# Optimization experiments

Measured on AMD Instinct MI355X. Metric: run time of the kernel, lower is better.

Reference implementation:

```python
import jax, jax.numpy as jnp
import numpy as np

B, S, HID = 4, 2048, 2048
NH, NKV, HD = 16, 4, 128  # query heads, kv heads, head_dim


def setup_inputs() -> dict:
    key = jax.random.key(0)
    ks = jax.random.split(key, 7)
    scale = 1.0 / np.sqrt(HID)
    x = jax.random.normal(ks[0], (B, S, HID), dtype=jnp.float32)
    # rope tables (interleaved-pair convention matching rotate_half)
    inv_freq = 1.0 / (1000000.0 ** (np.arange(0, HD, 2, dtype=np.float32) / HD))
    t = np.arange(S, dtype=np.float32)
    freqs = np.outer(t, inv_freq)                      # (S, HD/2)
    emb = np.repeat(freqs, 2, axis=-1)                 # (S, HD) interleaved
    cos = jnp.asarray(np.cos(emb))
    sin = jnp.asarray(np.sin(emb))
    wq = jax.random.normal(ks[1], (HID, NH * HD), dtype=jnp.float32) * scale
    wk = jax.random.normal(ks[2], (HID, NKV * HD), dtype=jnp.float32) * scale
    wv = jax.random.normal(ks[3], (HID, NKV * HD), dtype=jnp.float32) * scale
    wo = jax.random.normal(ks[4], (NH * HD, HID), dtype=jnp.float32) * scale
    return {"x": x, "cos": cos, "sin": sin, "wq": wq, "wk": wk, "wv": wv, "wo": wo}


def _rotate_half(u):
    even = u[..., ::2]
    odd = u[..., 1::2]
    return jnp.stack((-odd, even), axis=-1).reshape(u.shape)


def reference(x, cos, sin, wq, wk, wv, wo):
    b, s, _ = x.shape
    rep = NH // NKV
    q = (x @ wq).reshape(b, s, NH, HD)
    k = (x @ wk).reshape(b, s, NKV, HD)
    v = (x @ wv).reshape(b, s, NKV, HD)
    # RoPE: cos/sin (S, HD) -> broadcast over batch and heads (unsqueeze_dim=1)
    c = cos[:s][None, :, None, :]
    sn = sin[:s][None, :, None, :]
    q = q * c + _rotate_half(q) * sn
    k = k * c + _rotate_half(k) * sn
    # GQA: group query heads per kv head; avoid materializing repeated K/V
    q = q.transpose(0, 2, 1, 3).reshape(b, NKV, rep, s, HD)   # (b, kv, rep, s, d)
    k = k.transpose(0, 2, 1, 3)                                # (b, kv, s, d)
    v = v.transpose(0, 2, 1, 3)                                # (b, kv, s, d)
    scores = jnp.einsum("bgrqd,bgkd->bgrqk", q, k) / jnp.sqrt(jnp.float32(HD))
    causal = jnp.tril(jnp.ones((s, s), dtype=bool))
    scores = jnp.where(causal, scores, jnp.finfo(scores.dtype).min)
    probs = jax.nn.softmax(scores, axis=-1)
    out = jnp.einsum("bgrqk,bgkd->bgrqd", probs, v)            # (b, kv, rep, s, d)
    out = out.reshape(b, NH, s, HD).transpose(0, 2, 1, 3).reshape(b, s, NH * HD)
    return out @ wo
```

## Files before the change

kernel.cpp:

```cpp
#include <hip/hip_runtime.h>

#define HIDD 2048
#define SEQ  2048
#define BATCH 4
#define NHQ  16
#define NKVH 4
#define HDIM 128
#define QKVN 3072

typedef unsigned short u16;
typedef unsigned int   u32;
using bf16x8 = __attribute__((ext_vector_type(8))) __bf16;
using u16x8  = __attribute__((ext_vector_type(8))) u16;
using u16x4  = __attribute__((ext_vector_type(4))) u16;
using f32x4  = __attribute__((ext_vector_type(4))) float;

__device__ __forceinline__ float bf2f(u16 v){ u32 u = ((u32)v) << 16; float f; __builtin_memcpy(&f, &u, 4); return f; }
__device__ __forceinline__ u16 f2bf(float f){ u32 u; __builtin_memcpy(&u, &f, 4); u += 0x7fffu + ((u >> 16) & 1u); return (u16)(u >> 16); }

__device__ __forceinline__ void gl_lds16(const void* g, void* l){
  __builtin_amdgcn_global_load_lds((const __attribute__((address_space(1))) void*)g,
                                   (__attribute__((address_space(3))) void*)l, 16, 0, 0);
}


__global__ void cvt_f32_bf16(const float* __restrict__ in, u16* __restrict__ out, int n4){
  int i = blockIdx.x * 256 + threadIdx.x;
  if (i >= n4) return;
  float4 v = ((const float4*)in)[i];
  u16x4 o; o[0] = f2bf(v.x); o[1] = f2bf(v.y); o[2] = f2bf(v.z); o[3] = f2bf(v.w);
  ((u16x4*)out)[i] = o;
}

__global__ void transpose_cvt_f32(const float* __restrict__ in, u16* __restrict__ out, int R, int C){
  __shared__ float t[32][33];
  int c0 = blockIdx.x * 32, r0 = blockIdx.y * 32;
  int tx = threadIdx.x, ty = threadIdx.y;
  #pragma unroll
  for (int i = 0; i < 4; i++)
    t[ty + 8*i][tx] = in[(size_t)(r0 + ty + 8*i) * C + c0 + tx];
  __syncthreads();
  #pragma unroll
  for (int i = 0; i < 4; i++)
    out[(size_t)(c0 + ty + 8*i) * R + r0 + tx] = f2bf(t[tx][ty + 8*i]);
}

__global__ void transpose_v(const u16* __restrict__ V, u16* __restrict__ Vt, int ld, int voff){
  __shared__ u16 t[32][33];
  int bg = blockIdx.z;
  int b = bg >> 2, g = bg & 3;
  const u16* in = V + (size_t)b * SEQ * ld + voff + g * HDIM;
  u16* out = Vt + (size_t)bg * HDIM * SEQ;
  int c0 = blockIdx.x * 32, r0 = blockIdx.y * 32;
  int tx = threadIdx.x, ty = threadIdx.y;
  #pragma unroll
  for (int i = 0; i < 4; i++)
    t[ty + 8*i][tx] = in[(size_t)(r0 + ty + 8*i) * ld + c0 + tx];
  __syncthreads();
  #pragma unroll
  for (int i = 0; i < 4; i++)
    out[(size_t)(c0 + ty + 8*i) * SEQ + r0 + tx] = t[tx][ty + 8*i];
}

__global__ void rope_kernel(u16* __restrict__ X, int ld, int ncl,
                            const float* __restrict__ ct, const float* __restrict__ st,
                            float scale, int n8){
  int i = blockIdx.x * 256 + threadIdx.x;
  if (i >= n8) return;
  int e0 = i * 8;
  int row = e0 >> ncl;
  int col = e0 & ((1 << ncl) - 1);
  int pos = row & (SEQ - 1);
  int dd  = col & (HDIM - 1);
  u16* p = X + (size_t)row * ld + col;
  u16x8 v = *(const u16x8*)p;
  const float* cp = ct + (size_t)pos * HDIM + dd;
  const float* sp = st + (size_t)pos * HDIM + dd;
  float f[8];
  #pragma unroll
  for (int j = 0; j < 8; j++) f[j] = bf2f(v[j]);
  u16x8 o;
  #pragma unroll
  for (int j = 0; j < 8; j += 2){
    float c = cp[j], s = sp[j];
    float e = f[j], od = f[j+1];
    o[j]   = f2bf((e * c - od * s) * scale);
    o[j+1] = f2bf((od * c + e * s) * scale);
  }
  *(u16x8*)p = o;
}

template<int OUT_BF16>
__global__ __launch_bounds__(256) void gemm_bt(const u16* __restrict__ A, const u16* __restrict__ Bt,
                                               void* __restrict__ Cv, int M, int N, int K){
  __shared__ __align__(16) u16 As[128*32];
  __shared__ __align__(16) u16 Bs[128*32];
  const int tid = threadIdx.x;
  const int wid = tid >> 6, lane = tid & 63;
  const int lr = lane & 15, lk = lane >> 4;
  const int m0 = blockIdx.y * 128, n0 = blockIdx.x * 128;
  const int wr = (wid >> 1) * 64, wc = (wid & 1) * 64;

  f32x4 acc[4][4];
  #pragma unroll
  for (int m = 0; m < 4; m++)
    #pragma unroll
    for (int n = 0; n < 4; n++) acc[m][n] = f32x4{0.f,0.f,0.f,0.f};

  const int srow = lane >> 2;
  const int swz  = ((lane & 3) * 8) ^ ((srow & 3) * 8);
  const u16* Ag = A  + (size_t)(m0 + wid*32 + srow) * K + swz;
  const u16* Bg = Bt + (size_t)(n0 + wid*32 + srow) * K + swz;
  u16* Asl = As + wid * 1024;
  u16* Bsl = Bs + wid * 1024;
  const int rsw = (lr & 3) * 8;

  for (int k0 = 0; k0 < K; k0 += 32){
    gl_lds16(Ag + k0,          Asl);
    gl_lds16(Ag + k0 + 16*K,   Asl + 512);
    gl_lds16(Bg + k0,          Bsl);
    gl_lds16(Bg + k0 + 16*K,   Bsl + 512);
    __syncthreads();
    bf16x8 a[4], b[4];
    #pragma unroll
    for (int m = 0; m < 4; m++) a[m] = *(const bf16x8*)&As[(wr + m*16 + lr)*32 + ((lk*8) ^ rsw)];
    #pragma unroll
    for (int n = 0; n < 4; n++) b[n] = *(const bf16x8*)&Bs[(wc + n*16 + lr)*32 + ((lk*8) ^ rsw)];
    #pragma unroll
    for (int m = 0; m < 4; m++)
      #pragma unroll
      for (int n = 0; n < 4; n++)
        acc[m][n] = __builtin_amdgcn_mfma_f32_16x16x32_bf16(a[m], b[n], acc[m][n], 0, 0, 0);
    __syncthreads();
  }
  #pragma unroll
  for (int m = 0; m < 4; m++)
    #pragma unroll
    for (int n = 0; n < 4; n++)
      #pragma unroll
      for (int i = 0; i < 4; i++){
        int gr = m0 + wr + m*16 + lk*4 + i;
        int gc = n0 + wc + n*16 + lr;
        float v = acc[m][n][i];
        if (OUT_BF16) ((u16*)Cv)[(size_t)gr * N + gc] = f2bf(v);
        else          ((float*)Cv)[(size_t)gr * N + gc] = v;
      }
}

__global__ __launch_bounds__(256) void attn_kernel(const u16* __restrict__ QKV, const u16* __restrict__ Vt,
                                                   u16* __restrict__ O){
  const int qt = (gridDim.x - 1) - blockIdx.x;
  const int h = blockIdx.y, b = blockIdx.z;
  const int g = h >> 2;
  const int tid = threadIdx.x;
  const int wid = tid >> 6, lane = tid & 63;
  const int lr = lane & 15, lk = lane >> 4;
  const int q0 = qt * 64;

  __shared__ __align__(16) u16 Ks[2][64*128];
  __shared__ __align__(16) u16 Vs[2][128*64];
  __shared__ __align__(16) u16 Ps[4][16*72];

  bf16x8 qf[4];
  {
    const int qrow = q0 + wid*16 + lr;
    const u16* qp = QKV + (size_t)(b*SEQ + qrow) * QKVN + h*HDIM + lk*8;
    #pragma unroll
    for (int c = 0; c < 4; c++) qf[c] = *(const bf16x8*)(qp + c*32);
  }

  const u16* Kbase = QKV + (size_t)b * SEQ * QKVN + HIDD + g*HDIM;
  const u16* Vbase = Vt + (size_t)(b*NKVH + g) * HDIM * SEQ;
  const int klr = lane >> 4, kj = lane & 15;
  const int vlr = lane >> 3, vj = lane & 7;

  #define STAGE(buf, t) do {                                                        \
    int kv0_ = (t) * 64;                                                            \
    _Pragma("unroll")                                                               \
    for (int iw = 0; iw < 4; iw++){                                                 \
      int kcb = wid*4 + iw;                                                         \
      int r   = kcb*4 + klr;                                                        \
      gl_lds16(Kbase + (size_t)(kv0_ + r) * QKVN + ((kj ^ (r & 7)) << 3),           \
               &Ks[buf][kcb << 9]);                                                 \
      int d   = kcb*8 + vlr;                                                        \
      gl_lds16(Vbase + (size_t)d * SEQ + kv0_ + ((vj ^ (d & 7)) << 3),              \
               &Vs[buf][kcb << 9]);                                                 \
    }                                                                               \
  } while (0)

  f32x4 oacc[8];
  #pragma unroll
  for (int f = 0; f < 8; f++) oacc[f] = f32x4{0.f,0.f,0.f,0.f};
  float m_i[4], l_i[4];
  #pragma unroll
  for (int i = 0; i < 4; i++){ m_i[i] = -1e30f; l_i[i] = 0.f; }

  const int nt = qt + 1;
  int cur = 0;
  STAGE(0, 0);
  for (int t = 0; t < nt; ++t){
    __syncthreads();
    if (t + 1 < nt) STAGE(cur ^ 1, t + 1);

    const int kv0 = t * 64;
    f32x4 sf[4];
    #pragma unroll
    for (int n = 0; n < 4; n++){
      f32x4 a = f32x4{0.f,0.f,0.f,0.f};
      #pragma unroll
      for (int c = 0; c < 4; c++){
        bf16x8 kf = *(const bf16x8*)&Ks[cur][(n*16 + lr)*128 + (((c*4 + lk) ^ (lr & 7)) << 3)];
        a = __builtin_amdgcn_mfma_f32_16x16x32_bf16(qf[c], kf, a, 0, 0, 0);
      }
      sf[n] = a;
    }
    if (t == nt - 1){
      #pragma unroll
      for (int n = 0; n < 4; n++)
        #pragma unroll
        for (int i = 0; i < 4; i++){
          int kvg = kv0 + n*16 + lr;
          int qg  = q0 + wid*16 + lk*4 + i;
          if (kvg > qg) sf[n][i] = -1e30f;
        }
    }
    float rm[4];
    #pragma unroll
    for (int i = 0; i < 4; i++) rm[i] = fmaxf(fmaxf(sf[0][i], sf[1][i]), fmaxf(sf[2][i], sf[3][i]));
    #pragma unroll
    for (int off = 1; off < 16; off <<= 1)
      #pragma unroll
      for (int i = 0; i < 4; i++) rm[i] = fmaxf(rm[i], __shfl_xor(rm[i], off));

    int defer = 1;
    #pragma unroll
    for (int i = 0; i < 4; i++) defer &= (rm[i] <= m_i[i] + 11.5f);

    float p[4][4], rs[4];
    if (__all(defer)){
      #pragma unroll
      for (int i = 0; i < 4; i++){
        float s0 = 0.f;
        #pragma unroll
        for (int n = 0; n < 4; n++){ float pv = exp2f(sf[n][i] - m_i[i]); p[n][i] = pv; s0 += pv; }
        rs[i] = s0;
      }
    } else {
      #pragma unroll
      for (int i = 0; i < 4; i++){
        float mn = fmaxf(m_i[i], rm[i]);
        float cf = exp2f(m_i[i] - mn);
        float s0 = 0.f;
        #pragma unroll
        for (int n = 0; n < 4; n++){ float pv = exp2f(sf[n][i] - mn); p[n][i] = pv; s0 += pv; }
        rs[i] = s0; m_i[i] = mn; l_i[i] *= cf;
        #pragma unroll
        for (int f = 0; f < 8; f++) oacc[f][i] *= cf;
      }
    }
    #pragma unroll
    for (int off = 1; off < 16; off <<= 1)
      #pragma unroll
      for (int i = 0; i < 4; i++) rs[i] += __shfl_xor(rs[i], off);
    #pragma unroll
    for (int i = 0; i < 4; i++) l_i[i] += rs[i];

    #pragma unroll
    for (int n = 0; n < 4; n++)
      #pragma unroll
      for (int i = 0; i < 4; i++)
        Ps[wid][(lk*4 + i)*72 + n*16 + lr] = f2bf(p[n][i]);

    #pragma unroll
    for (int kc = 0; kc < 2; kc++){
      bf16x8 pf = *(const bf16x8*)&Ps[wid][lr*72 + kc*32 + lk*8];
      #pragma unroll
      for (int f = 0; f < 8; f++){
        bf16x8 vf = *(const bf16x8*)&Vs[cur][(f*16 + lr)*64 + (((kc*4 + lk) ^ (lr & 7)) << 3)];
        oacc[f] = __builtin_amdgcn_mfma_f32_16x16x32_bf16(pf, vf, oacc[f], 0, 0, 0);
      }
    }
    cur ^= 1;
  }
  #undef STAGE
  #pragma unroll
  for (int f = 0; f < 8; f++)
    #pragma unroll
    for (int i = 0; i < 4; i++){
      int qr = q0 + wid*16 + lk*4 + i;
      float v = oacc[f][i] / l_i[i];
      O[(size_t)(b*SEQ + qr) * (NHQ*HDIM) + h*HDIM + f*16 + lr] = f2bf(v);
    }
}


extern "C" void kernel_launch(void* const* d_in, const int* in_sizes, int n_in,
                              void* d_out, int out_size, void* d_ws, size_t ws_size,
                              hipStream_t stream){
  const float* x    = (const float*)d_in[0];
  const float* cosb = (const float*)d_in[1];
  const float* sinb = (const float*)d_in[2];
  const float* wq   = (const float*)d_in[3];
  const float* wk   = (const float*)d_in[4];
  const float* wv   = (const float*)d_in[5];
  const float* wo   = (const float*)d_in[6];
  float* out = (float*)d_out;

  char* ws = (char*)d_ws;
  u16* XB    = (u16*)(ws);
  u16* WQKVT = (u16*)(ws + 33554432);
  u16* WOT   = (u16*)(ws + 46137344);
  u16* QKV   = (u16*)(ws + 54525952);
  u16* VT    = (u16*)(ws + 104857600);

  dim3 tb(32, 8);
  cvt_f32_bf16<<<(BATCH*SEQ*HIDD/4 + 255)/256, 256, 0, stream>>>(x, XB, BATCH*SEQ*HIDD/4);
  transpose_cvt_f32<<<dim3(HIDD/32, HIDD/32), tb, 0, stream>>>(wq, WQKVT, HIDD, NHQ*HDIM);
  transpose_cvt_f32<<<dim3((NKVH*HDIM)/32, HIDD/32), tb, 0, stream>>>(wk, WQKVT + (size_t)2048*2048, HIDD, NKVH*HDIM);
  transpose_cvt_f32<<<dim3((NKVH*HDIM)/32, HIDD/32), tb, 0, stream>>>(wv, WQKVT + (size_t)2560*2048, HIDD, NKVH*HDIM);
  transpose_cvt_f32<<<dim3(HIDD/32, HIDD/32), tb, 0, stream>>>(wo, WOT, NHQ*HDIM, HIDD);
  gemm_bt<1><<<dim3(QKVN/128, BATCH*SEQ/128), 256, 0, stream>>>(XB, WQKVT, QKV, BATCH*SEQ, QKVN, HIDD);
  rope_kernel<<<(BATCH*SEQ*2048/8)/256, 256, 0, stream>>>(QKV, QKVN, 11, cosb, sinb, 0.12753165651003169f, BATCH*SEQ*2048/8);
  rope_kernel<<<(BATCH*SEQ*512/8)/256, 256, 0, stream>>>(QKV + HIDD, QKVN, 9, cosb, sinb, 1.0f, BATCH*SEQ*512/8);
  transpose_v<<<dim3(HDIM/32, SEQ/32, BATCH*NKVH), tb, 0, stream>>>(QKV, VT, QKVN, 2560);
  attn_kernel<<<dim3(SEQ/64, NHQ, BATCH), 256, 0, stream>>>(QKV, VT, XB);
  gemm_bt<0><<<dim3(HIDD/128, BATCH*SEQ/128), 256, 0, stream>>>(XB, WOT, out, BATCH*SEQ, HIDD, NHQ*HDIM);
}
```

Baseline: 758.2 us.

## Enlarge attention query tile to 128 rows with two 16-row subtiles per wave

Each block now handles 128 query rows, and each wave handles 32 rows as two 16-row subtiles. Every K/V tile staged into LDS is therefore reused across twice as many queries, and the K fragments read from LDS are shared by both subtiles. The QK MFMA is transposed (K as the A operand) so each lane owns one query row, which reduces the row max and row sum to two cross-lane shuffles. K/V staging pointers are precomputed and incremented, and fully masked tiles are skipped per wave. In exchange the grid has half as many blocks, each wave holds more registers, and causal work is less balanced within a block.

```diff
diff --git a/kernel.cpp b/kernel.cpp
--- a/kernel.cpp
+++ b/kernel.cpp
@@ -155,142 +155,162 @@
   const int tid = threadIdx.x;
   const int wid = tid >> 6, lane = tid & 63;
   const int lr = lane & 15, lk = lane >> 4;
-  const int q0 = qt * 64;
+  const int q0 = qt * 128;
+  const int q0w = q0 + wid * 32;
 
   __shared__ __align__(16) u16 Ks[2][64*128];
   __shared__ __align__(16) u16 Vs[2][128*64];
   __shared__ __align__(16) u16 Ps[4][16*72];
-
-  bf16x8 qf[4];
-  {
-    const int qrow = q0 + wid*16 + lr;
-    const u16* qp = QKV + (size_t)(b*SEQ + qrow) * QKVN + h*HDIM + lk*8;
-    #pragma unroll
-    for (int c = 0; c < 4; c++) qf[c] = *(const bf16x8*)(qp + c*32);
-  }
-
-  const u16* Kbase = QKV + (size_t)b * SEQ * QKVN + HIDD + g*HDIM;
-  const u16* Vbase = Vt + (size_t)(b*NKVH + g) * HDIM * SEQ;
+  u16* Pw = &Ps[wid][0];
+
+  bf16x8 qf[2][4];
+  #pragma unroll
+  for (int qh = 0; qh < 2; qh++){
+    const u16* qp = QKV + (size_t)(b*SEQ + q0w + qh*16 + lr) * QKVN + h*HDIM + lk*8;
+    #pragma unroll
+    for (int c = 0; c < 4; c++) qf[qh][c] = *(const bf16x8*)(qp + c*32);
+  }
+
   const int klr = lane >> 4, kj = lane & 15;
   const int vlr = lane >> 3, vj = lane & 7;
-
-  #define STAGE(buf, t) do {                                                        \
-    int kv0_ = (t) * 64;                                                            \
-    _Pragma("unroll")                                                               \
-    for (int iw = 0; iw < 4; iw++){                                                 \
-      int kcb = wid*4 + iw;                                                         \
-      int r   = kcb*4 + klr;                                                        \
-      gl_lds16(Kbase + (size_t)(kv0_ + r) * QKVN + ((kj ^ (r & 7)) << 3),           \
-               &Ks[buf][kcb << 9]);                                                 \
-      int d   = kcb*8 + vlr;                                                        \
-      gl_lds16(Vbase + (size_t)d * SEQ + kv0_ + ((vj ^ (d & 7)) << 3),              \
-               &Vs[buf][kcb << 9]);                                                 \
-    }                                                                               \
-  } while (0)
-
-  f32x4 oacc[8];
-  #pragma unroll
-  for (int f = 0; f < 8; f++) oacc[f] = f32x4{0.f,0.f,0.f,0.f};
-  float m_i[4], l_i[4];
-  #pragma unroll
-  for (int i = 0; i < 4; i++){ m_i[i] = -1e30f; l_i[i] = 0.f; }
-
-  const int nt = qt + 1;
+  const u16* Kst[4]; const u16* Vst[4];
+  {
+    const u16* Kbase = QKV + (size_t)b * SEQ * QKVN + HIDD + g*HDIM;
+    const u16* Vbase = Vt + (size_t)(b*NKVH + g) * HDIM * SEQ;
+    #pragma unroll
+    for (int iw = 0; iw < 4; iw++){
+      int kcb = wid*4 + iw;
+      int r   = kcb*4 + klr;
+      Kst[iw] = Kbase + (size_t)r * QKVN + ((kj ^ (r & 7)) << 3);
+      int d   = kcb*8 + vlr;
+      Vst[iw] = Vbase + (size_t)d * SEQ + ((vj ^ (d & 7)) << 3);
+    }
+  }
+
+  f32x4 oacc[2][8];
+  #pragma unroll
+  for (int qh = 0; qh < 2; qh++)
+    #pragma unroll
+    for (int f = 0; f < 8; f++) oacc[qh][f] = f32x4{0.f,0.f,0.f,0.f};
+  float m_i[2] = {-1e30f, -1e30f}, l_i[2] = {0.f, 0.f};
+
+  const int nt = 2 * (qt + 1);
   int cur = 0;
-  STAGE(0, 0);
+  #pragma unroll
+  for (int iw = 0; iw < 4; iw++){
+    int kcb = wid*4 + iw;
+    gl_lds16(Kst[iw], &Ks[0][kcb << 9]);
+    gl_lds16(Vst[iw], &Vs[0][kcb << 9]);
+    Kst[iw] += 64 * QKVN;
+    Vst[iw] += 64;
+  }
+
   for (int t = 0; t < nt; ++t){
     __syncthreads();
-    if (t + 1 < nt) STAGE(cur ^ 1, t + 1);
-
+    if (t + 1 < nt){
+      #pragma unroll
+      for (int iw = 0; iw < 4; iw++){
+        int kcb = wid*4 + iw;
+        gl_lds16(Kst[iw], &Ks[cur ^ 1][kcb << 9]);
+        gl_lds16(Vst[iw], &Vs[cur ^ 1][kcb << 9]);
+        Kst[iw] += 64 * QKVN;
+        Vst[iw] += 64;
+      }
+    }
     const int kv0 = t * 64;
-    f32x4 sf[4];
-    #pragma unroll
-    for (int n = 0; n < 4; n++){
-      f32x4 a = f32x4{0.f,0.f,0.f,0.f};
-      #pragma unroll
-      for (int c = 0; c < 4; c++){
-        bf16x8 kf = *(const bf16x8*)&Ks[cur][(n*16 + lr)*128 + (((c*4 + lk) ^ (lr & 7)) << 3)];
-        a = __builtin_amdgcn_mfma_f32_16x16x32_bf16(qf[c], kf, a, 0, 0, 0);
-      }
-      sf[n] = a;
-    }
-    if (t == nt - 1){
-      #pragma unroll
-      for (int n = 0; n < 4; n++)
-        #pragma unroll
-        for (int i = 0; i < 4; i++){
-          int kvg = kv0 + n*16 + lr;
-          int qg  = q0 + wid*16 + lk*4 + i;
-          if (kvg > qg) sf[n][i] = -1e30f;
+    if (kv0 <= q0w + 31){
+      f32x4 sf[2][4];
+      #pragma unroll
+      for (int n = 0; n < 4; n++){
+        bf16x8 kf[4];
+        #pragma unroll
+        for (int c = 0; c < 4; c++)
+          kf[c] = *(const bf16x8*)&Ks[cur][(n*16 + lr)*128 + (((c*4 + lk) ^ (lr & 7)) << 3)];
+        #pragma unroll
+        for (int qh = 0; qh < 2; qh++){
+          f32x4 a = f32x4{0.f,0.f,0.f,0.f};
+          #pragma unroll
+          for (int c = 0; c < 4; c++)
+            a = __builtin_amdgcn_mfma_f32_16x16x32_bf16(kf[c], qf[qh][c], a, 0, 0, 0);
+          sf[qh][n] = a;
         }
-    }
-    float rm[4];
-    #pragma unroll
-    for (int i = 0; i < 4; i++) rm[i] = fmaxf(fmaxf(sf[0][i], sf[1][i]), fmaxf(sf[2][i], sf[3][i]));
-    #pragma unroll
-    for (int off = 1; off < 16; off <<= 1)
-      #pragma unroll
-      for (int i = 0; i < 4; i++) rm[i] = fmaxf(rm[i], __shfl_xor(rm[i], off));
-
-    int defer = 1;
-    #pragma unroll
-    for (int i = 0; i < 4; i++) defer &= (rm[i] <= m_i[i] + 11.5f);
-
-    float p[4][4], rs[4];
-    if (__all(defer)){
-      #pragma unroll
-      for (int i = 0; i < 4; i++){
-        float s0 = 0.f;
-        #pragma unroll
-        for (int n = 0; n < 4; n++){ float pv = exp2f(sf[n][i] - m_i[i]); p[n][i] = pv; s0 += pv; }
-        rs[i] = s0;
-      }
-    } else {
-      #pragma unroll
-      for (int i = 0; i < 4; i++){
-        float mn = fmaxf(m_i[i], rm[i]);
-        float cf = exp2f(m_i[i] - mn);
-        float s0 = 0.f;
-        #pragma unroll
-        for (int n = 0; n < 4; n++){ float pv = exp2f(sf[n][i] - mn); p[n][i] = pv; s0 += pv; }
-        rs[i] = s0; m_i[i] = mn; l_i[i] *= cf;
-        #pragma unroll
-        for (int f = 0; f < 8; f++) oacc[f][i] *= cf;
-      }
-    }
-    #pragma unroll
-    for (int off = 1; off < 16; off <<= 1)
-      #pragma unroll
-      for (int i = 0; i < 4; i++) rs[i] += __shfl_xor(rs[i], off);
-    #pragma unroll
-    for (int i = 0; i < 4; i++) l_i[i] += rs[i];
-
-    #pragma unroll
-    for (int n = 0; n < 4; n++)
-      #pragma unroll
-      for (int i = 0; i < 4; i++)
-        Ps[wid][(lk*4 + i)*72 + n*16 + lr] = f2bf(p[n][i]);
-
-    #pragma unroll
-    for (int kc = 0; kc < 2; kc++){
-      bf16x8 pf = *(const bf16x8*)&Ps[wid][lr*72 + kc*32 + lk*8];
-      #pragma unroll
-      for (int f = 0; f < 8; f++){
-        bf16x8 vf = *(const bf16x8*)&Vs[cur][(f*16 + lr)*64 + (((kc*4 + lk) ^ (lr & 7)) << 3)];
-        oacc[f] = __builtin_amdgcn_mfma_f32_16x16x32_bf16(pf, vf, oacc[f], 0, 0, 0);
+      }
+      if (kv0 + 63 > q0w){
+        #pragma unroll
+        for (int qh = 0; qh < 2; qh++)
+          #pragma unroll
+          for (int n = 0; n < 4; n++)
+            #pragma unroll
+            for (int i = 0; i < 4; i++){
+              int kvg = kv0 + n*16 + lk*4 + i;
+              int qg  = q0w + qh*16 + lr;
+              if (kvg > qg) sf[qh][n][i] = -1e30f;
+            }
+      }
+      #pragma unroll
+      for (int qh = 0; qh < 2; qh++){
+        float rm = sf[qh][0][0];
+        #pragma unroll
+        for (int n = 0; n < 4; n++)
+          #pragma unroll
+          for (int i = 0; i < 4; i++) rm = fmaxf(rm, sf[qh][n][i]);
+        rm = fmaxf(rm, __shfl_xor(rm, 16));
+        rm = fmaxf(rm, __shfl_xor(rm, 32));
+
+        if (!__all(rm <= m_i[qh] + 11.5f)){
+          float mn = fmaxf(m_i[qh], rm);
+          float cf = exp2f(m_i[qh] - mn);
+          m_i[qh] = mn; l_i[qh] *= cf;
+          float cfq[4];
+          #pragma unroll
+          for (int i = 0; i < 4; i++) cfq[i] = __shfl(cf, lk*4 + i);
+          #pragma unroll
+          for (int f = 0; f < 8; f++)
+            #pragma unroll
+            for (int i = 0; i < 4; i++) oacc[qh][f][i] *= cfq[i];
+        }
+        float rs = 0.f;
+        #pragma unroll
+        for (int n = 0; n < 4; n++){
+          u16x4 pp;
+          #pragma unroll
+          for (int i = 0; i < 4; i++){
+            float pv = exp2f(sf[qh][n][i] - m_i[qh]);
+            rs += pv;
+            pp[i] = f2bf(pv);
+          }
+          *(u16x4*)&Pw[lr*72 + n*16 + lk*4] = pp;
+        }
+        rs += __shfl_xor(rs, 16);
+        rs += __shfl_xor(rs, 32);
+        l_i[qh] += rs;
+
+        #pragma unroll
+        for (int kc = 0; kc < 2; kc++){
+          bf16x8 pf = *(const bf16x8*)&Pw[lr*72 + kc*32 + lk*8];
+          #pragma unroll
+          for (int f = 0; f < 8; f++){
+            bf16x8 vf = *(const bf16x8*)&Vs[cur][(f*16 + lr)*64 + (((kc*4 + lk) ^ (lr & 7)) << 3)];
+            oacc[qh][f] = __builtin_amdgcn_mfma_f32_16x16x32_bf16(pf, vf, oacc[qh][f], 0, 0, 0);
+          }
+        }
       }
     }
     cur ^= 1;
   }
-  #undef STAGE
-  #pragma unroll
-  for (int f = 0; f < 8; f++)
-    #pragma unroll
-    for (int i = 0; i < 4; i++){
-      int qr = q0 + wid*16 + lk*4 + i;
-      float v = oacc[f][i] / l_i[i];
-      O[(size_t)(b*SEQ + qr) * (NHQ*HDIM) + h*HDIM + f*16 + lr] = f2bf(v);
-    }
+  #pragma unroll
+  for (int qh = 0; qh < 2; qh++){
+    float linv[4];
+    #pragma unroll
+    for (int i = 0; i < 4; i++) linv[i] = 1.0f / __shfl(l_i[qh], lk*4 + i);
+    #pragma unroll
+    for (int f = 0; f < 8; f++)
+      #pragma unroll
+      for (int i = 0; i < 4; i++){
+        int qr = q0w + qh*16 + lk*4 + i;
+        O[(size_t)(b*SEQ + qr) * (NHQ*HDIM) + h*HDIM + f*16 + lr] = f2bf(oacc[qh][f][i] * linv[i]);
+      }
+  }
 }
 
 
@@ -323,6 +343,6 @@
   rope_kernel<<<(BATCH*SEQ*2048/8)/256, 256, 0, stream>>>(QKV, QKVN, 11, cosb, sinb, 0.12753165651003169f, BATCH*SEQ*2048/8);
   rope_kernel<<<(BATCH*SEQ*512/8)/256, 256, 0, stream>>>(QKV + HIDD, QKVN, 9, cosb, sinb, 1.0f, BATCH*SEQ*512/8);
   transpose_v<<<dim3(HDIM/32, SEQ/32, BATCH*NKVH), tb, 0, stream>>>(QKV, VT, QKVN, 2560);
-  attn_kernel<<<dim3(SEQ/64, NHQ, BATCH), 256, 0, stream>>>(QKV, VT, XB);
+  attn_kernel<<<dim3(SEQ/128, NHQ, BATCH), 256, 0, stream>>>(QKV, VT, XB);
   gemm_bt<0><<<dim3(HIDD/128, BATCH*SEQ/128), 256, 0, stream>>>(XB, WOT, out, BATCH*SEQ, HIDD, NHQ*HDIM);
 }
```

After: 761.5 us. No clear change (+0.4%).
